# Kernel tuning notes

Measured on AMD Instinct MI355X. Metric: run time of the kernel, lower is better.

## Reference

```python
import jax, jax.numpy as jnp
import numpy as np

HIDDEN = 4096
N_HEADS = 32
N_KV_HEADS = 8
HEAD_DIM = HIDDEN // N_HEADS  # 128
ROPE_THETA = 10000.0


def rotate_half(x):
    x1, x2 = jnp.split(x, 2, axis=-1)
    return jnp.concatenate((-x2, x1), axis=-1)


def rope_cos_sin(seq_len, dim, theta, dtype):
    inv_freq = 1.0 / (theta ** (jnp.arange(0, dim, 2, dtype=jnp.float32) / dim))
    t = jnp.arange(seq_len, dtype=jnp.float32)
    freqs = jnp.outer(t, inv_freq)               # [S, D/2]
    emb = jnp.concatenate((freqs, freqs), axis=-1)  # [S, D]
    return jnp.cos(emb).astype(dtype), jnp.sin(emb).astype(dtype)


def setup_inputs() -> dict:
    key = jax.random.key(0)
    k0, k1, k2, k3, k4 = jax.random.split(key, 5)
    B, S = 1, 2048
    std = 1.0 / np.sqrt(HIDDEN)
    return {
        "hidden_states": jax.random.normal(k0, (B, S, HIDDEN), dtype=jnp.float32),
        "wq": jax.random.normal(k1, (N_HEADS * HEAD_DIM, HIDDEN), dtype=jnp.float32) * std,
        "wk": jax.random.normal(k2, (N_KV_HEADS * HEAD_DIM, HIDDEN), dtype=jnp.float32) * std,
        "wv": jax.random.normal(k3, (N_KV_HEADS * HEAD_DIM, HIDDEN), dtype=jnp.float32) * std,
        "wo": jax.random.normal(k4, (HIDDEN, N_HEADS * HEAD_DIM), dtype=jnp.float32) * std,
    }


def reference(hidden_states, wq, wk, wv, wo):
    B, S, _ = hidden_states.shape
    dtype = hidden_states.dtype
    G = N_HEADS // N_KV_HEADS  # query groups per kv head

    # projections (torch Linear: x @ W.T)
    q = (hidden_states @ wq.T).reshape(B, S, N_HEADS, HEAD_DIM).transpose(0, 2, 1, 3)      # [B,H,S,D]
    k = (hidden_states @ wk.T).reshape(B, S, N_KV_HEADS, HEAD_DIM).transpose(0, 2, 1, 3)   # [B,Hkv,S,D]
    v = (hidden_states @ wv.T).reshape(B, S, N_KV_HEADS, HEAD_DIM).transpose(0, 2, 1, 3)   # [B,Hkv,S,D]

    cos, sin = rope_cos_sin(S, HEAD_DIM, ROPE_THETA, dtype)  # [S,D]
    cos = cos[None, None]  # [1,1,S,D]
    sin = sin[None, None]
    q = q * cos + rotate_half(q) * sin
    k = k * cos + rotate_half(k) * sin

    # GQA: group query heads with their kv head (equivalent to repeat_interleave on kv)
    qg = q.reshape(B, N_KV_HEADS, G, S, HEAD_DIM)
    scale = 1.0 / np.sqrt(HEAD_DIM)
    scores = jnp.einsum("bkgsd,bktd->bkgst", qg, k) * scale  # [B,Hkv,G,S,S]

    causal = jnp.tril(jnp.ones((S, S), dtype=bool))
    scores = jnp.where(causal, scores, -jnp.inf)
    probs = jax.nn.softmax(scores.astype(jnp.float32), axis=-1).astype(dtype)

    out = jnp.einsum("bkgst,bktd->bkgsd", probs, v)  # [B,Hkv,G,S,D]
    out = out.reshape(B, N_HEADS, S, HEAD_DIM).transpose(0, 2, 1, 3).reshape(B, S, N_HEADS * HEAD_DIM)
    return out @ wo.T
```

## Files before the change

kernel.cpp:

```cpp
#include <hip/hip_runtime.h>
#include <hip/hip_bf16.h>


typedef _Float16 half4_t __attribute__((ext_vector_type(4)));
typedef _Float16 half8_t __attribute__((ext_vector_type(8)));
typedef float f32x4 __attribute__((ext_vector_type(4)));

#define S_LEN 2048
#define HID 4096
#define NH 32
#define NKV 8

__device__ __forceinline__ void gload_lds16(const void* g, void* l) {
  __builtin_amdgcn_global_load_lds((const __attribute__((address_space(1))) void*)g,
                                   (__attribute__((address_space(3))) void*)l, 16, 0, 0);
}

__global__ __launch_bounds__(256) void cvt_f32_f16(const float* __restrict__ src,
                                                   _Float16* __restrict__ dst, int n4) {
  int i = blockIdx.x * 256 + threadIdx.x;
  if (i >= n4) return;
  f32x4 v = *(const f32x4*)(src + (size_t)i * 4);
  half4_t h = {(_Float16)v[0], (_Float16)v[1], (_Float16)v[2], (_Float16)v[3]};
  *(half4_t*)(dst + (size_t)i * 4) = h;
}

__global__ __launch_bounds__(256) void rope_table_kernel(float* __restrict__ cost,
                                                         float* __restrict__ sint) {
  int i = blockIdx.x * 256 + threadIdx.x;
  int d = i & 63;
  int s = i >> 6;
  float inv = exp2f(-(float)d * (13.287712379549449f / 64.0f));
  float f = (float)s * inv;
  cost[i] = cosf(f);
  sint[i] = sinf(f);
}

__global__ __launch_bounds__(256) void rope_apply_q(_Float16* __restrict__ X,
                                                    const float* __restrict__ cost,
                                                    const float* __restrict__ sint) {
  int idx = blockIdx.x * 256 + threadIdx.x;
  int g = idx & 15;
  int tmp = idx >> 4;
  int h = tmp % NH;
  int s = tmp / NH;
  int d0 = g * 4;
  size_t base = (size_t)s * HID + h * 128 + d0;
  half4_t x1 = *(half4_t*)(X + base);
  half4_t x2 = *(half4_t*)(X + base + 64);
  const float* cp = cost + s * 64 + d0;
  const float* sp = sint + s * 64 + d0;
  half4_t y1, y2;
#pragma unroll
  for (int j = 0; j < 4; ++j) {
    float c = cp[j], sn = sp[j];
    float a = (float)x1[j], b = (float)x2[j];
    y1[j] = (_Float16)(a * c - b * sn);
    y2[j] = (_Float16)(b * c + a * sn);
  }
  *(half4_t*)(X + base) = y1;
  *(half4_t*)(X + base + 64) = y2;
}

__global__ __launch_bounds__(256) void rope_apply_k2(const _Float16* __restrict__ Kin,
                                                     const float* __restrict__ cost,
                                                     const float* __restrict__ sint,
                                                     _Float16* __restrict__ K2) {
  int idx = blockIdx.x * 256 + threadIdx.x;
  int g = idx & 15;
  int tmp = idx >> 4;
  int h = tmp % NKV;
  int s = tmp / NKV;
  int d0 = g * 4;
  size_t base = (size_t)s * (NKV * 128) + h * 128 + d0;
  half4_t x1 = *(const half4_t*)(Kin + base);
  half4_t x2 = *(const half4_t*)(Kin + base + 64);
  const float* cp = cost + s * 64 + d0;
  const float* sp = sint + s * 64 + d0;
  half4_t y1, y2;
#pragma unroll
  for (int j = 0; j < 4; ++j) {
    float c = cp[j], sn = sp[j];
    float a = (float)x1[j], b = (float)x2[j];
    y1[j] = (_Float16)(a * c - b * sn);
    y2[j] = (_Float16)(b * c + a * sn);
  }
  size_t tb = (size_t)h * (S_LEN * 128) + (size_t)(s >> 4) * 2048 + (size_t)(s & 15) * 8;
  int d1 = d0, d2 = d0 + 64;
  *(half4_t*)(K2 + tb + (d1 >> 3) * 128 + (d1 & 7)) = y1;
  *(half4_t*)(K2 + tb + (d2 >> 3) * 128 + (d2 & 7)) = y2;
}

template <int MODE>
__global__ __launch_bounds__(256) void gemm_h(const _Float16* __restrict__ A,
                                              const _Float16* __restrict__ W,
                                              void* __restrict__ Cout,
                                              int M, int N, int K) {
  __shared__ __align__(16) _Float16 As[128 * 32];
  __shared__ __align__(16) _Float16 Bs[128 * 32];
  const int t = threadIdx.x, w = t >> 6, l = t & 63, lr = l & 15, lg = l >> 4;
  const int m0 = blockIdx.y * 128, n0 = blockIdx.x * 128;
  const int wm = (w >> 1) * 64, wn = (w & 1) * 64;
  const int srow = l >> 2, scol = (l & 3) * 8;
  f32x4 acc[4][4] = {};
  const _Float16* ap = A + (size_t)m0 * K + scol;
  const _Float16* bp = W + (size_t)n0 * K + scol;

  for (int kb = 0; kb < K; kb += 32) {
#pragma unroll
    for (int it = 0; it < 2; ++it) {
      const int ci = it * 4 + w;
      const int r = ci * 16 + srow;
      gload_lds16(ap + (size_t)r * K + kb, As + ci * 512);
      gload_lds16(bp + (size_t)r * K + kb, Bs + ci * 512);
    }
    __syncthreads();
    half8_t af[4], bf[4];
#pragma unroll
    for (int mi = 0; mi < 4; ++mi)
      af[mi] = *(const half8_t*)(As + (wm + mi * 16 + lr) * 32 + lg * 8);
#pragma unroll
    for (int ni = 0; ni < 4; ++ni)
      bf[ni] = *(const half8_t*)(Bs + (wn + ni * 16 + lr) * 32 + lg * 8);
#pragma unroll
    for (int mi = 0; mi < 4; ++mi)
#pragma unroll
      for (int ni = 0; ni < 4; ++ni)
        acc[mi][ni] = __builtin_amdgcn_mfma_f32_16x16x32_f16(af[mi], bf[ni], acc[mi][ni], 0, 0, 0);
    __syncthreads();
  }

#pragma unroll
  for (int mi = 0; mi < 4; ++mi) {
#pragma unroll
    for (int ni = 0; ni < 4; ++ni) {
      int row = m0 + wm + mi * 16 + lg * 4;
      int col = n0 + wn + ni * 16 + lr;
#pragma unroll
      for (int i = 0; i < 4; ++i) {
        if (MODE == 1)
          ((float*)Cout)[(size_t)(row + i) * N + col] = acc[mi][ni][i];
        else
          ((_Float16*)Cout)[(size_t)(row + i) * N + col] = (_Float16)acc[mi][ni][i];
      }
    }
  }
}

__global__ __launch_bounds__(256) void gemm_kv(const _Float16* __restrict__ A,
                                               const _Float16* __restrict__ Wk,
                                               const _Float16* __restrict__ Wv,
                                               _Float16* __restrict__ Ck,
                                               _Float16* __restrict__ V2) {
  __shared__ __align__(16) _Float16 As[128 * 32];
  __shared__ __align__(16) _Float16 Bs[128 * 32];
  const int K = HID;
  const int t = threadIdx.x, w = t >> 6, l = t & 63, lr = l & 15, lg = l >> 4;
  const bool isv = blockIdx.x >= 8;
  const int m0 = blockIdx.y * 128, n0 = (blockIdx.x & 7) * 128;
  const _Float16* W = isv ? Wv : Wk;
  const int wm = (w >> 1) * 64, wn = (w & 1) * 64;
  const int srow = l >> 2, scol = (l & 3) * 8;
  f32x4 acc[4][4] = {};
  const _Float16* ap = A + (size_t)m0 * K + scol;
  const _Float16* bp = W + (size_t)n0 * K + scol;

  for (int kb = 0; kb < K; kb += 32) {
#pragma unroll
    for (int it = 0; it < 2; ++it) {
      const int ci = it * 4 + w;
      const int r = ci * 16 + srow;
      gload_lds16(ap + (size_t)r * K + kb, As + ci * 512);
      gload_lds16(bp + (size_t)r * K + kb, Bs + ci * 512);
    }
    __syncthreads();
    half8_t af[4], bf[4];
#pragma unroll
    for (int mi = 0; mi < 4; ++mi)
      af[mi] = *(const half8_t*)(As + (wm + mi * 16 + lr) * 32 + lg * 8);
#pragma unroll
    for (int ni = 0; ni < 4; ++ni)
      bf[ni] = *(const half8_t*)(Bs + (wn + ni * 16 + lr) * 32 + lg * 8);
#pragma unroll
    for (int mi = 0; mi < 4; ++mi)
#pragma unroll
      for (int ni = 0; ni < 4; ++ni)
        acc[mi][ni] = __builtin_amdgcn_mfma_f32_16x16x32_f16(af[mi], bf[ni], acc[mi][ni], 0, 0, 0);
    __syncthreads();
  }

#pragma unroll
  for (int mi = 0; mi < 4; ++mi) {
#pragma unroll
    for (int ni = 0; ni < 4; ++ni) {
      int row = m0 + wm + mi * 16 + lg * 4;
      int col = n0 + wn + ni * 16 + lr;
      if (!isv) {
#pragma unroll
        for (int i = 0; i < 4; ++i)
          Ck[(size_t)(row + i) * (NKV * 128) + col] = (_Float16)acc[mi][ni][i];
      } else {
        half4_t o;
#pragma unroll
        for (int i = 0; i < 4; ++i) o[i] = (_Float16)acc[mi][ni][i];
        *(half4_t*)(V2 + (size_t)(col >> 7) * (S_LEN * 128) + (size_t)(row >> 4) * 2048 +
                    (size_t)(col & 127) * 16 + (row & 15)) = o;
      }
    }
  }
}

__global__ __launch_bounds__(256) void attn_kernel(const _Float16* __restrict__ Q,
                                                   const _Float16* __restrict__ K2,
                                                   const _Float16* __restrict__ V2,
                                                   _Float16* __restrict__ Op,
                                                   float* __restrict__ Md) {
  const int bid = blockIdx.x;
  const int hk = bid & 7;
  const int split = (bid >> 3) & 1;
  const int qt = 63 - (bid >> 4);
  const int w = threadIdx.x >> 6;
  const int h = hk * 4 + w;
  const int l = threadIdx.x & 63;
  const int lr = l & 15;
  const int lg = l >> 4;
  const float scale = 0.08838834764831845f;
  const float LOG2E = 1.4426950408889634f;
  const float NEG = -1.0e30f;

  const int half_steps = qt + 1;
  const int kt0 = split * half_steps;
  const int kt1 = kt0 + half_steps;

  int sq[2];
  half8_t qf[2][4];
#pragma unroll
  for (int qc = 0; qc < 2; ++qc) {
    sq[qc] = qt * 32 + qc * 16 + lr;
#pragma unroll
    for (int c = 0; c < 4; ++c)
      qf[qc][c] = *(const half8_t*)(Q + (size_t)sq[qc] * HID + h * 128 + c * 32 + lg * 8);
  }
  const _Float16* Kb = K2 + (size_t)hk * (S_LEN * 128);
  const _Float16* Vb = V2 + (size_t)hk * (S_LEN * 128);

  f32x4 acc[8][2] = {};
  float m[2] = {NEG, NEG};
  float den[2] = {0.f, 0.f};

  for (int kt = kt0; kt < kt1; ++kt) {
    half8_t kf[4];
#pragma unroll
    for (int c = 0; c < 4; ++c)
      kf[c] = *(const half8_t*)(Kb + (size_t)kt * 2048 + (c * 4 + lg) * 128 + lr * 8);
    f32x4 s0 = {0.f, 0.f, 0.f, 0.f}, s1 = {0.f, 0.f, 0.f, 0.f};
#pragma unroll
    for (int c = 0; c < 4; ++c) {
      s0 = __builtin_amdgcn_mfma_f32_16x16x32_f16(kf[c], qf[0][c], s0, 0, 0, 0);
      s1 = __builtin_amdgcn_mfma_f32_16x16x32_f16(kf[c], qf[1][c], s1, 0, 0, 0);
    }
    const int kbase = kt * 16 + lg * 4;
    float sc[2][4];
#pragma unroll
    for (int i = 0; i < 4; ++i) {
      sc[0][i] = s0[i] * scale;
      sc[1][i] = s1[i] * scale;
    }
    if (kt >= 2 * qt) {
#pragma unroll
      for (int qc = 0; qc < 2; ++qc)
#pragma unroll
        for (int i = 0; i < 4; ++i)
          if (kbase + i > sq[qc]) sc[qc][i] = NEG;
    }
    half4_t pf[2];
#pragma unroll
    for (int qc = 0; qc < 2; ++qc) {
      float mx = fmaxf(fmaxf(sc[qc][0], sc[qc][1]), fmaxf(sc[qc][2], sc[qc][3]));
      mx = fmaxf(mx, __shfl_xor(mx, 16));
      mx = fmaxf(mx, __shfl_xor(mx, 32));
      if (!__all(mx - m[qc] <= 8.0f)) {
        float mn = fmaxf(m[qc], mx);
        float corr = exp2f((m[qc] - mn) * LOG2E);
        den[qc] *= corr;
#pragma unroll
        for (int dc = 0; dc < 8; ++dc)
#pragma unroll
          for (int i = 0; i < 4; ++i) acc[dc][qc][i] *= corr;
        m[qc] = mn;
      }
      float ps = 0.f, p[4];
#pragma unroll
      for (int i = 0; i < 4; ++i) {
        p[i] = exp2f((sc[qc][i] - m[qc]) * LOG2E);
        ps += p[i];
      }
      ps += __shfl_xor(ps, 16);
      ps += __shfl_xor(ps, 32);
      den[qc] += ps;
      pf[qc] = (half4_t){(_Float16)p[0], (_Float16)p[1], (_Float16)p[2], (_Float16)p[3]};
    }
#pragma unroll
    for (int dc = 0; dc < 8; ++dc) {
      half4_t vf = *(const half4_t*)(Vb + (size_t)kt * 2048 + (dc * 16 + lr) * 16 + lg * 4);
      acc[dc][0] = __builtin_amdgcn_mfma_f32_16x16x16f16(vf, pf[0], acc[dc][0], 0, 0, 0);
      acc[dc][1] = __builtin_amdgcn_mfma_f32_16x16x16f16(vf, pf[1], acc[dc][1], 0, 0, 0);
    }
  }

  _Float16* Os = Op + (size_t)split * S_LEN * HID;
#pragma unroll
  for (int qc = 0; qc < 2; ++qc) {
    float inv = den[qc] > 0.f ? 1.0f / den[qc] : 0.f;
#pragma unroll
    for (int dc = 0; dc < 8; ++dc) {
      half4_t o;
#pragma unroll
      for (int i = 0; i < 4; ++i) o[i] = (_Float16)(acc[dc][qc][i] * inv);
      *(half4_t*)(Os + (size_t)sq[qc] * HID + h * 128 + dc * 16 + lg * 4) = o;
    }
    if (lg == 0) {
      int mdix = ((split * S_LEN + sq[qc]) * NH + h) * 2;
      Md[mdix] = m[qc];
      Md[mdix + 1] = den[qc];
    }
  }
}

__global__ __launch_bounds__(256) void attn_combine(const _Float16* __restrict__ Op,
                                                    const float* __restrict__ Md,
                                                    _Float16* __restrict__ O) {
  const float LOG2E = 1.4426950408889634f;
  int idx = blockIdx.x * 256 + threadIdx.x;
  int dd = (idx & 15) * 8;
  int h = (idx >> 4) & 31;
  int s = idx >> 9;
  int base = (s * NH + h) * 2;
  float m0 = Md[base], den0 = Md[base + 1];
  float m1 = Md[S_LEN * NH * 2 + base], den1 = Md[S_LEN * NH * 2 + base + 1];
  float M = fmaxf(m0, m1);
  float w0 = den0 * exp2f((m0 - M) * LOG2E);
  float w1 = den1 * exp2f((m1 - M) * LOG2E);
  float r = 1.0f / (w0 + w1);
  w0 *= r;
  w1 *= r;
  size_t off = (size_t)s * HID + h * 128 + dd;
  half8_t a = *(const half8_t*)(Op + off);
  half8_t b = *(const half8_t*)(Op + (size_t)S_LEN * HID + off);
  half8_t o;
#pragma unroll
  for (int j = 0; j < 8; ++j) o[j] = (_Float16)(w0 * (float)a[j] + w1 * (float)b[j]);
  *(half8_t*)(O + off) = o;
}

extern "C" void kernel_launch(void* const* d_in, const int* in_sizes, int n_in,
                              void* d_out, int out_size, void* d_ws, size_t ws_size,
                              hipStream_t stream) {
  (void)in_sizes; (void)n_in; (void)out_size; (void)ws_size;
  const float* hs = (const float*)d_in[0];
  const float* wq = (const float*)d_in[1];
  const float* wk = (const float*)d_in[2];
  const float* wv = (const float*)d_in[3];
  const float* wo = (const float*)d_in[4];

  char* ws = (char*)d_ws;
  _Float16* hs_h = (_Float16*)(ws);
  _Float16* K2   = hs_h;
  _Float16* q_h  = (_Float16*)(ws + (16u << 20));
  _Float16* k_h  = (_Float16*)(ws + (32u << 20));
  _Float16* V2   = (_Float16*)(ws + (36u << 20));
  float* cost    = (float*)(ws + (40u << 20));
  float* sint    = (float*)(ws + (40u << 20) + (512u << 10));
  _Float16* wbuf = (_Float16*)(ws + (41u << 20));
  _Float16* wbuf2 = wbuf + (8u << 20) / 2;
  _Float16* Op   = wbuf;
  float* Md      = (float*)(ws + (73u << 20));
  _Float16* o_h  = hs_h;

  cvt_f32_f16<<<8192, 256, 0, stream>>>(hs, hs_h, (S_LEN * HID) / 4);
  rope_table_kernel<<<(S_LEN * 64) / 256, 256, 0, stream>>>(cost, sint);

  cvt_f32_f16<<<16384, 256, 0, stream>>>(wq, wbuf, (HID * HID) / 4);
  gemm_h<0><<<dim3(32, 16), 256, 0, stream>>>(hs_h, wbuf, q_h, S_LEN, HID, HID);

  cvt_f32_f16<<<4096, 256, 0, stream>>>(wk, wbuf, (NKV * 128 * HID) / 4);
  cvt_f32_f16<<<4096, 256, 0, stream>>>(wv, wbuf2, (NKV * 128 * HID) / 4);
  gemm_kv<<<dim3(16, 16), 256, 0, stream>>>(hs_h, wbuf, wbuf2, k_h, V2);

  rope_apply_q<<<(S_LEN * NH * 16) / 256, 256, 0, stream>>>(q_h, cost, sint);
  rope_apply_k2<<<(S_LEN * NKV * 16) / 256, 256, 0, stream>>>(k_h, cost, sint, K2);

  attn_kernel<<<1024, 256, 0, stream>>>(q_h, K2, V2, Op, Md);
  attn_combine<<<4096, 256, 0, stream>>>(Op, Md, o_h);

  cvt_f32_f16<<<16384, 256, 0, stream>>>(wo, wbuf, (HID * HID) / 4);
  gemm_h<1><<<dim3(32, 16), 256, 0, stream>>>(o_h, wbuf, d_out, S_LEN, HID, HID);
}
```

Before: 447.9 us.

## Merge QKV projections into one double-buffered GEMM with swizzled block order

Replaces the separate Q and KV projection GEMMs with a single templated GEMM that covers Q, K and V columns in one launch when enough workspace is available. The new kernel double-buffers its LDS tiles and remaps block indices into an interleaved order. K is written straight into the tiled K2 layout, and RoPE is then applied to it in place, which removes the intermediate row-major K buffer. The aim is to cut launch count, improve load/compute overlap and L2 reuse, at the cost of doubled LDS use and scattered 2-byte K2 stores.

```diff
diff --git a/kernel.cpp b/kernel.cpp
--- a/kernel.cpp
+++ b/kernel.cpp
@@ -62,19 +62,20 @@
   *(half4_t*)(X + base + 64) = y2;
 }
 
-__global__ __launch_bounds__(256) void rope_apply_k2(const _Float16* __restrict__ Kin,
-                                                     const float* __restrict__ cost,
-                                                     const float* __restrict__ sint,
-                                                     _Float16* __restrict__ K2) {
+__global__ __launch_bounds__(256) void rope_k2_inplace(_Float16* __restrict__ K2,
+                                                       const float* __restrict__ cost,
+                                                       const float* __restrict__ sint) {
   int idx = blockIdx.x * 256 + threadIdx.x;
   int g = idx & 15;
   int tmp = idx >> 4;
   int h = tmp % NKV;
   int s = tmp / NKV;
   int d0 = g * 4;
-  size_t base = (size_t)s * (NKV * 128) + h * 128 + d0;
-  half4_t x1 = *(const half4_t*)(Kin + base);
-  half4_t x2 = *(const half4_t*)(Kin + base + 64);
+  size_t tb = (size_t)h * (S_LEN * 128) + (size_t)(s >> 4) * 2048 + (size_t)(s & 15) * 8;
+  size_t a1 = tb + (size_t)(d0 >> 3) * 128 + (d0 & 7);
+  size_t a2 = a1 + 1024;
+  half4_t x1 = *(half4_t*)(K2 + a1);
+  half4_t x2 = *(half4_t*)(K2 + a2);
   const float* cp = cost + s * 64 + d0;
   const float* sp = sint + s * 64 + d0;
   half4_t y1, y2;
@@ -85,120 +86,95 @@
     y1[j] = (_Float16)(a * c - b * sn);
     y2[j] = (_Float16)(b * c + a * sn);
   }
-  size_t tb = (size_t)h * (S_LEN * 128) + (size_t)(s >> 4) * 2048 + (size_t)(s & 15) * 8;
-  int d1 = d0, d2 = d0 + 64;
-  *(half4_t*)(K2 + tb + (d1 >> 3) * 128 + (d1 & 7)) = y1;
-  *(half4_t*)(K2 + tb + (d2 >> 3) * 128 + (d2 & 7)) = y2;
+  *(half4_t*)(K2 + a1) = y1;
+  *(half4_t*)(K2 + a2) = y2;
 }
 
 template <int MODE>
-__global__ __launch_bounds__(256) void gemm_h(const _Float16* __restrict__ A,
-                                              const _Float16* __restrict__ W,
-                                              void* __restrict__ Cout,
-                                              int M, int N, int K) {
-  __shared__ __align__(16) _Float16 As[128 * 32];
-  __shared__ __align__(16) _Float16 Bs[128 * 32];
+__global__ __launch_bounds__(256) void gemm5(const _Float16* __restrict__ A,
+                                             const _Float16* __restrict__ W0,
+                                             const _Float16* __restrict__ W1,
+                                             const _Float16* __restrict__ W2,
+                                             void* __restrict__ out,
+                                             _Float16* __restrict__ K2,
+                                             _Float16* __restrict__ V2, int bxoff) {
+  __shared__ __align__(16) _Float16 As[2][128 * 32];
+  __shared__ __align__(16) _Float16 Bs[2][128 * 32];
   const int t = threadIdx.x, w = t >> 6, l = t & 63, lr = l & 15, lg = l >> 4;
-  const int m0 = blockIdx.y * 128, n0 = blockIdx.x * 128;
+  const int nwg = gridDim.x * gridDim.y;
+  const int flat = blockIdx.y * gridDim.x + blockIdx.x;
+  const int rm = (flat & 7) * (nwg >> 3) + (flat >> 3);
+  const int bx = rm % gridDim.x + bxoff;
+  const int by = rm / gridDim.x;
+  const int m0 = by * 128;
+  const _Float16* Wsel;
+  int col0, sel;
+  if (MODE == 1) {
+    Wsel = W0; col0 = bx * 128; sel = 0;
+  } else {
+    if (bx < 32)      { Wsel = W0; col0 = bx * 128; sel = 0; }
+    else if (bx < 40) { Wsel = W1; col0 = (bx - 32) * 128; sel = 1; }
+    else              { Wsel = W2; col0 = (bx - 40) * 128; sel = 2; }
+  }
   const int wm = (w >> 1) * 64, wn = (w & 1) * 64;
   const int srow = l >> 2, scol = (l & 3) * 8;
+  const _Float16* ap = A + (size_t)m0 * 4096 + scol;
+  const _Float16* bp = Wsel + (size_t)col0 * 4096 + scol;
   f32x4 acc[4][4] = {};
-  const _Float16* ap = A + (size_t)m0 * K + scol;
-  const _Float16* bp = W + (size_t)n0 * K + scol;
-
-  for (int kb = 0; kb < K; kb += 32) {
-#pragma unroll
-    for (int it = 0; it < 2; ++it) {
-      const int ci = it * 4 + w;
-      const int r = ci * 16 + srow;
-      gload_lds16(ap + (size_t)r * K + kb, As + ci * 512);
-      gload_lds16(bp + (size_t)r * K + kb, Bs + ci * 512);
-    }
-    __syncthreads();
+
+#define STAGE5(as_, bs_, kb_)                                     \
+  _Pragma("unroll") for (int it = 0; it < 2; ++it) {              \
+    const int ci = it * 4 + w;                                    \
+    const int r = ci * 16 + srow;                                 \
+    gload_lds16(ap + (size_t)r * 4096 + (kb_), (as_) + ci * 512); \
+    gload_lds16(bp + (size_t)r * 4096 + (kb_), (bs_) + ci * 512); \
+  }
+
+  STAGE5(As[0], Bs[0], 0)
+  __syncthreads();
+  int cur = 0;
+  for (int kb = 0; kb < 4096; kb += 32) {
+    if (kb + 32 < 4096) {
+      STAGE5(As[cur ^ 1], Bs[cur ^ 1], kb + 32)
+    }
     half8_t af[4], bf[4];
 #pragma unroll
     for (int mi = 0; mi < 4; ++mi)
-      af[mi] = *(const half8_t*)(As + (wm + mi * 16 + lr) * 32 + lg * 8);
+      af[mi] = *(const half8_t*)(As[cur] + (wm + mi * 16 + lr) * 32 + lg * 8);
 #pragma unroll
     for (int ni = 0; ni < 4; ++ni)
-      bf[ni] = *(const half8_t*)(Bs + (wn + ni * 16 + lr) * 32 + lg * 8);
+      bf[ni] = *(const half8_t*)(Bs[cur] + (wn + ni * 16 + lr) * 32 + lg * 8);
 #pragma unroll
     for (int mi = 0; mi < 4; ++mi)
 #pragma unroll
       for (int ni = 0; ni < 4; ++ni)
         acc[mi][ni] = __builtin_amdgcn_mfma_f32_16x16x32_f16(af[mi], bf[ni], acc[mi][ni], 0, 0, 0);
     __syncthreads();
-  }
+    cur ^= 1;
+  }
+#undef STAGE5
 
 #pragma unroll
   for (int mi = 0; mi < 4; ++mi) {
 #pragma unroll
     for (int ni = 0; ni < 4; ++ni) {
-      int row = m0 + wm + mi * 16 + lg * 4;
-      int col = n0 + wn + ni * 16 + lr;
-#pragma unroll
-      for (int i = 0; i < 4; ++i) {
-        if (MODE == 1)
-          ((float*)Cout)[(size_t)(row + i) * N + col] = acc[mi][ni][i];
-        else
-          ((_Float16*)Cout)[(size_t)(row + i) * N + col] = (_Float16)acc[mi][ni][i];
-      }
-    }
-  }
-}
-
-__global__ __launch_bounds__(256) void gemm_kv(const _Float16* __restrict__ A,
-                                               const _Float16* __restrict__ Wk,
-                                               const _Float16* __restrict__ Wv,
-                                               _Float16* __restrict__ Ck,
-                                               _Float16* __restrict__ V2) {
-  __shared__ __align__(16) _Float16 As[128 * 32];
-  __shared__ __align__(16) _Float16 Bs[128 * 32];
-  const int K = HID;
-  const int t = threadIdx.x, w = t >> 6, l = t & 63, lr = l & 15, lg = l >> 4;
-  const bool isv = blockIdx.x >= 8;
-  const int m0 = blockIdx.y * 128, n0 = (blockIdx.x & 7) * 128;
-  const _Float16* W = isv ? Wv : Wk;
-  const int wm = (w >> 1) * 64, wn = (w & 1) * 64;
-  const int srow = l >> 2, scol = (l & 3) * 8;
-  f32x4 acc[4][4] = {};
-  const _Float16* ap = A + (size_t)m0 * K + scol;
-  const _Float16* bp = W + (size_t)n0 * K + scol;
-
-  for (int kb = 0; kb < K; kb += 32) {
-#pragma unroll
-    for (int it = 0; it < 2; ++it) {
-      const int ci = it * 4 + w;
-      const int r = ci * 16 + srow;
-      gload_lds16(ap + (size_t)r * K + kb, As + ci * 512);
-      gload_lds16(bp + (size_t)r * K + kb, Bs + ci * 512);
-    }
-    __syncthreads();
-    half8_t af[4], bf[4];
-#pragma unroll
-    for (int mi = 0; mi < 4; ++mi)
-      af[mi] = *(const half8_t*)(As + (wm + mi * 16 + lr) * 32 + lg * 8);
-#pragma unroll
-    for (int ni = 0; ni < 4; ++ni)
-      bf[ni] = *(const half8_t*)(Bs + (wn + ni * 16 + lr) * 32 + lg * 8);
-#pragma unroll
-    for (int mi = 0; mi < 4; ++mi)
-#pragma unroll
-      for (int ni = 0; ni < 4; ++ni)
-        acc[mi][ni] = __builtin_amdgcn_mfma_f32_16x16x32_f16(af[mi], bf[ni], acc[mi][ni], 0, 0, 0);
-    __syncthreads();
-  }
-
-#pragma unroll
-  for (int mi = 0; mi < 4; ++mi) {
-#pragma unroll
-    for (int ni = 0; ni < 4; ++ni) {
-      int row = m0 + wm + mi * 16 + lg * 4;
-      int col = n0 + wn + ni * 16 + lr;
-      if (!isv) {
+      const int row = m0 + wm + mi * 16 + lg * 4;
+      const int col = col0 + wn + ni * 16 + lr;
+      if (MODE == 1) {
 #pragma unroll
         for (int i = 0; i < 4; ++i)
-          Ck[(size_t)(row + i) * (NKV * 128) + col] = (_Float16)acc[mi][ni][i];
+          ((float*)out)[(size_t)(row + i) * 4096 + col] = acc[mi][ni][i];
+      } else if (sel == 0) {
+#pragma unroll
+        for (int i = 0; i < 4; ++i)
+          ((_Float16*)out)[(size_t)(row + i) * 4096 + col] = (_Float16)acc[mi][ni][i];
+      } else if (sel == 1) {
+        const int h = col >> 7, d = col & 127;
+        const size_t kb2 = (size_t)h * (S_LEN * 128) + (size_t)(row >> 4) * 2048 +
+                           (size_t)(d >> 3) * 128 + (d & 7);
+#pragma unroll
+        for (int i = 0; i < 4; ++i)
+          K2[kb2 + ((row + i) & 15) * 8] = (_Float16)acc[mi][ni][i];
       } else {
         half4_t o;
 #pragma unroll
@@ -356,7 +332,7 @@
 extern "C" void kernel_launch(void* const* d_in, const int* in_sizes, int n_in,
                               void* d_out, int out_size, void* d_ws, size_t ws_size,
                               hipStream_t stream) {
-  (void)in_sizes; (void)n_in; (void)out_size; (void)ws_size;
+  (void)in_sizes; (void)n_in; (void)out_size;
   const float* hs = (const float*)d_in[0];
   const float* wq = (const float*)d_in[1];
   const float* wk = (const float*)d_in[2];
@@ -365,14 +341,12 @@
 
   char* ws = (char*)d_ws;
   _Float16* hs_h = (_Float16*)(ws);
-  _Float16* K2   = hs_h;
-  _Float16* q_h  = (_Float16*)(ws + (16u << 20));
-  _Float16* k_h  = (_Float16*)(ws + (32u << 20));
+  _Float16* K2   = (_Float16*)(ws + (32u << 20));
   _Float16* V2   = (_Float16*)(ws + (36u << 20));
   float* cost    = (float*)(ws + (40u << 20));
   float* sint    = (float*)(ws + (40u << 20) + (512u << 10));
+  _Float16* q_h  = (_Float16*)(ws + (16u << 20));
   _Float16* wbuf = (_Float16*)(ws + (41u << 20));
-  _Float16* wbuf2 = wbuf + (8u << 20) / 2;
   _Float16* Op   = wbuf;
   float* Md      = (float*)(ws + (73u << 20));
   _Float16* o_h  = hs_h;
@@ -380,19 +354,30 @@
   cvt_f32_f16<<<8192, 256, 0, stream>>>(hs, hs_h, (S_LEN * HID) / 4);
   rope_table_kernel<<<(S_LEN * 64) / 256, 256, 0, stream>>>(cost, sint);
 
-  cvt_f32_f16<<<16384, 256, 0, stream>>>(wq, wbuf, (HID * HID) / 4);
-  gemm_h<0><<<dim3(32, 16), 256, 0, stream>>>(hs_h, wbuf, q_h, S_LEN, HID, HID);
-
-  cvt_f32_f16<<<4096, 256, 0, stream>>>(wk, wbuf, (NKV * 128 * HID) / 4);
-  cvt_f32_f16<<<4096, 256, 0, stream>>>(wv, wbuf2, (NKV * 128 * HID) / 4);
-  gemm_kv<<<dim3(16, 16), 256, 0, stream>>>(hs_h, wbuf, wbuf2, k_h, V2);
+  const bool merged = ws_size >= (90ull << 20);
+  if (merged) {
+    _Float16* wk_h = (_Float16*)(ws + (73u << 20));
+    _Float16* wv_h = (_Float16*)(ws + (81u << 20));
+    cvt_f32_f16<<<16384, 256, 0, stream>>>(wq, wbuf, (HID * HID) / 4);
+    cvt_f32_f16<<<4096, 256, 0, stream>>>(wk, wk_h, (NKV * 128 * HID) / 4);
+    cvt_f32_f16<<<4096, 256, 0, stream>>>(wv, wv_h, (NKV * 128 * HID) / 4);
+    gemm5<0><<<dim3(48, 16), 256, 0, stream>>>(hs_h, wbuf, wk_h, wv_h, q_h, K2, V2, 0);
+  } else {
+    _Float16* wk_h = wbuf;
+    _Float16* wv_h = wbuf + (8u << 20) / 2;
+    cvt_f32_f16<<<16384, 256, 0, stream>>>(wq, wbuf, (HID * HID) / 4);
+    gemm5<0><<<dim3(32, 16), 256, 0, stream>>>(hs_h, wbuf, nullptr, nullptr, q_h, K2, V2, 0);
+    cvt_f32_f16<<<4096, 256, 0, stream>>>(wk, wk_h, (NKV * 128 * HID) / 4);
+    cvt_f32_f16<<<4096, 256, 0, stream>>>(wv, wv_h, (NKV * 128 * HID) / 4);
+    gemm5<0><<<dim3(16, 16), 256, 0, stream>>>(hs_h, nullptr, wk_h, wv_h, q_h, K2, V2, 32);
+  }
 
   rope_apply_q<<<(S_LEN * NH * 16) / 256, 256, 0, stream>>>(q_h, cost, sint);
-  rope_apply_k2<<<(S_LEN * NKV * 16) / 256, 256, 0, stream>>>(k_h, cost, sint, K2);
+  rope_k2_inplace<<<(S_LEN * NKV * 16) / 256, 256, 0, stream>>>(K2, cost, sint);
 
   attn_kernel<<<1024, 256, 0, stream>>>(q_h, K2, V2, Op, Md);
   attn_combine<<<4096, 256, 0, stream>>>(Op, Md, o_h);
 
   cvt_f32_f16<<<16384, 256, 0, stream>>>(wo, wbuf, (HID * HID) / 4);
-  gemm_h<1><<<dim3(32, 16), 256, 0, stream>>>(o_h, wbuf, d_out, S_LEN, HID, HID);
-}
+  gemm5<1><<<dim3(32, 16), 256, 0, stream>>>(o_h, wbuf, nullptr, nullptr, d_out, nullptr, nullptr, 0);
+}
```

Result: faster. 402.1 us (-10.2%).
